# Kernel tuning notes

Hardware: AMD Instinct MI355X
Metric: run time of the kernel (lower is better)

Reference implementation:

```python
import jax, jax.numpy as jnp
import numpy as np

N_NODES = 50000
NEG_SLOPE = 0.2

def _gat_conv(x, W, att_src, att_dst, bias, src, dst):
    # x: [N, in_c] -> h: [N, out_c]
    h = x @ W
    a_src = (h * att_src).sum(-1)  # [N]
    a_dst = (h * att_dst).sum(-1)  # [N]
    e = a_src[src] + a_dst[dst]    # [E]
    e = jnp.where(e > 0, e, NEG_SLOPE * e)  # LeakyReLU
    # segment softmax over destination node neighborhoods
    emax = jax.ops.segment_max(e, dst, num_segments=N_NODES)
    ee = jnp.exp(e - emax[dst])
    denom = jax.ops.segment_sum(ee, dst, num_segments=N_NODES)
    alpha = ee / denom[dst]        # [E]
    out = jax.ops.segment_sum(h[src] * alpha[:, None], dst, num_segments=N_NODES)
    return out + bias

def _with_self_loops(edge_index):
    # PyG GATConv default add_self_loops=True
    loop = jnp.arange(N_NODES, dtype=edge_index.dtype)
    src = jnp.concatenate([edge_index[0], loop])
    dst = jnp.concatenate([edge_index[1], loop])
    return src, dst

def setup_inputs() -> dict:
    key = jax.random.key(0)
    ks = jax.random.split(key, 11)
    in_c, hid_c, out_c = 256, 128, 64
    E = 800000
    x = jax.random.normal(ks[0], (N_NODES, in_c), dtype=jnp.float32)
    edge_index = jax.random.randint(ks[1], (2, E), 0, N_NODES, dtype=jnp.int64)
    s1 = 1.0 / np.sqrt(in_c)
    s2 = 1.0 / np.sqrt(hid_c)
    return {
        "x": x,
        "edge_index": edge_index,
        "W1": jax.random.normal(ks[2], (in_c, hid_c), dtype=jnp.float32) * s1,
        "att_src1": jax.random.normal(ks[3], (hid_c,), dtype=jnp.float32) * s2,
        "att_dst1": jax.random.normal(ks[4], (hid_c,), dtype=jnp.float32) * s2,
        "b1": jax.random.normal(ks[5], (hid_c,), dtype=jnp.float32) * 0.01,
        "W2": jax.random.normal(ks[6], (hid_c, out_c), dtype=jnp.float32) * s2,
        "att_src2": jax.random.normal(ks[7], (out_c,), dtype=jnp.float32) * (1.0 / np.sqrt(out_c)),
        "att_dst2": jax.random.normal(ks[8], (out_c,), dtype=jnp.float32) * (1.0 / np.sqrt(out_c)),
        "b2": jax.random.normal(ks[9], (out_c,), dtype=jnp.float32) * 0.01,
    }

def reference(x, edge_index, W1, att_src1, att_dst1, b1, W2, att_src2, att_dst2, b2):
    src, dst = _with_self_loops(edge_index)
    hid = _gat_conv(x, W1, att_src1, att_dst1, b1, src, dst)
    hid = jax.nn.relu(hid)
    out = _gat_conv(hid, W2, att_src2, att_dst2, b2, src, dst)
    return jax.nn.log_softmax(out, axis=1)
```

## Files before the change

### kernel.cpp

```cpp
#include <hip/hip_runtime.h>
#include <hip/hip_bf16.h>
#include <math.h>

#define N_NODES 50000
#define E_RAW   800000
#define E_TOT   850000
#define NEG_SLOPE 0.2f
#define CAP 64

typedef __attribute__((ext_vector_type(8))) short short8;
typedef __attribute__((ext_vector_type(4))) float f32x4;

__device__ __forceinline__ short f2bf(float f) {
    __hip_bfloat16 h = __float2bfloat16(f);
    return *reinterpret_cast<short*>(&h);
}
__device__ __forceinline__ unsigned int f2bfu(float f) {
    __hip_bfloat16 h = __float2bfloat16(f);
    return (unsigned int)*reinterpret_cast<unsigned short*>(&h);
}
__device__ __forceinline__ float bflo(unsigned int u) {
    return __uint_as_float(u << 16);
}
__device__ __forceinline__ float bfhi(unsigned int u) {
    return __uint_as_float(u & 0xffff0000u);
}

template<int K, int N>
__global__ __launch_bounds__(256) void gat_wf_kernel(
        const float* __restrict__ W, short* __restrict__ Wf) {
    constexpr int NT = N / 16;
    const int idx = blockIdx.x * 256 + threadIdx.x;
    if (idx >= K * N) return;
    const int j  = idx & 7;
    const int n  = (idx >> 3) & 15;
    const int q  = (idx >> 7) & 3;
    const int t  = (idx >> 9) % NT;
    const int kc = idx / (512 * NT);
    const int k   = kc * 32 + q * 8 + j;
    const int col = t * 16 + n;
    Wf[idx] = f2bf(W[(size_t)k * N + col]);
}

template<int K, int N, bool BF16_IN>
__device__ __forceinline__ void gemm_att_body(
        const int blk,
        const float* __restrict__ xf, const short* __restrict__ xb,
        const short* __restrict__ Wf,
        const float* __restrict__ att_src, const float* __restrict__ att_dst,
        short* __restrict__ h_bf,
        float* __restrict__ a_src, float* __restrict__ a_dst) {
    constexpr int NT = N / 16;
    constexpr int KC = K / 32;
    const int tid  = threadIdx.x;
    const int lane = tid & 63;
    const int wv   = tid >> 6;
    const int mrow = lane & 15;
    const int q    = lane >> 4;

    const int row0 = blk * 64 + wv * 16;
    const int rowA = row0 + mrow;
    const int rowAc = rowA < N_NODES ? rowA : 0;

    f32x4 acc[NT];
    #pragma unroll
    for (int t = 0; t < NT; ++t) acc[t] = f32x4{0.f, 0.f, 0.f, 0.f};

    #pragma unroll
    for (int kc = 0; kc < KC; ++kc) {
        short8 a;
        if (BF16_IN) {
            a = *(const short8*)&xb[(size_t)rowAc * K + kc * 32 + q * 8];
        } else {
            const float4 f0 = *(const float4*)&xf[(size_t)rowAc * K + kc * 32 + q * 8];
            const float4 f1 = *(const float4*)&xf[(size_t)rowAc * K + kc * 32 + q * 8 + 4];
            a[0] = f2bf(f0.x); a[1] = f2bf(f0.y); a[2] = f2bf(f0.z); a[3] = f2bf(f0.w);
            a[4] = f2bf(f1.x); a[5] = f2bf(f1.y); a[6] = f2bf(f1.z); a[7] = f2bf(f1.w);
        }
        #pragma unroll
        for (int t = 0; t < NT; ++t) {
            const short8 b = *(const short8*)&Wf[((size_t)(kc * NT + t) * 64 + lane) * 8];
            acc[t] = __builtin_amdgcn_mfma_f32_16x16x32_bf16(a, b, acc[t], 0, 0, 0);
        }
    }

    #pragma unroll
    for (int r = 0; r < 4; ++r) {
        const int rowD = row0 + q * 4 + r;
        float ps = 0.0f, pd = 0.0f;
        #pragma unroll
        for (int t = 0; t < NT; ++t) {
            const int col = t * 16 + mrow;
            ps = fmaf(acc[t][r], att_src[col], ps);
            pd = fmaf(acc[t][r], att_dst[col], pd);
        }
        #pragma unroll
        for (int off = 8; off > 0; off >>= 1) {
            ps += __shfl_xor(ps, off);
            pd += __shfl_xor(pd, off);
        }
        if (rowD < N_NODES) {
            if (mrow == 0) { a_src[rowD] = ps; a_dst[rowD] = pd; }
            #pragma unroll
            for (int t = 0; t < NT; ++t)
                h_bf[(size_t)rowD * N + t * 16 + mrow] = f2bf(acc[t][r]);
        }
    }
}

template<int K, int N>
__global__ __launch_bounds__(256) void gat_fat1_kernel(
        const float* __restrict__ xf, const short* __restrict__ Wf,
        const float* __restrict__ att_src, const float* __restrict__ att_dst,
        short* __restrict__ h_bf,
        float* __restrict__ a_src, float* __restrict__ a_dst,
        const int* __restrict__ ei, int* __restrict__ cnt,
        int* __restrict__ srcs, int GB) {
    if ((int)blockIdx.x < GB) {
        gemm_att_body<K, N, false>(blockIdx.x, xf, nullptr, Wf,
                                   att_src, att_dst, h_bf, a_src, a_dst);
    } else {
        const int i = (blockIdx.x - GB) * 256 + threadIdx.x;
        if (i >= E_TOT) return;
        int s, d;
        if (i < E_RAW) { s = ei[i]; d = ei[E_RAW + i]; }
        else           { s = d = i - E_RAW; }
        const int c = atomicAdd(&cnt[d], 1);
        if (c < CAP) srcs[(d << 6) + c] = s;
    }
}

template<int K, int N, bool BF16_IN>
__global__ __launch_bounds__(256) void gat_gemm_att_kernel(
        const float* __restrict__ xf, const short* __restrict__ xb,
        const short* __restrict__ Wf,
        const float* __restrict__ att_src, const float* __restrict__ att_dst,
        short* __restrict__ h_bf,
        float* __restrict__ a_src, float* __restrict__ a_dst) {
    gemm_att_body<K, N, BF16_IN>(blockIdx.x, xf, xb, Wf,
                                 att_src, att_dst, h_bf, a_src, a_dst);
}

template<int N, bool RELU, bool LSM, bool OUT_BF16>
__global__ __launch_bounds__(256) void gat_aggr_kernel(
        const int* __restrict__ cnt, const int* __restrict__ srcs,
        const float* __restrict__ a_src, const float* __restrict__ a_dst,
        const unsigned short* __restrict__ h_bf, const float* __restrict__ bias,
        float* __restrict__ outf, uint4* __restrict__ outb) {
    constexpr int EPL = N / 16;
    const int lane = threadIdx.x & 63;
    const int wave = threadIdx.x >> 6;
    const int d = blockIdx.x * 4 + wave;
    if (d >= N_NODES) return;
    const int beg = d << 6;
    int deg = cnt[d];
    deg = deg < CAP ? deg : CAP;
    const float ad = a_dst[d];

    const int sreg = srcs[beg + (lane < deg ? lane : 0)];
    float e;
    if (lane < deg) {
        float t = a_src[sreg] + ad;
        e = t > 0.0f ? t : NEG_SLOPE * t;
    } else {
        e = -1e30f;
    }
    float m = e;
    #pragma unroll
    for (int off = 32; off > 0; off >>= 1) m = fmaxf(m, __shfl_xor(m, off));
    const float anum = __expf(e - m);
    float ss = anum;
    #pragma unroll
    for (int off = 32; off > 0; off >>= 1) ss += __shfl_xor(ss, off);
    const float areg = anum / ss;

    const int g   = lane >> 4;
    const int sub = lane & 15;
    float acc[EPL];
    #pragma unroll
    for (int c = 0; c < EPL; ++c) acc[c] = 0.0f;

    for (int j = 0; j < deg; j += 4) {
        const int eidx = j + g;
        const int s    = __shfl(sreg, eidx);
        float alpha    = __shfl(areg, eidx);
        if (eidx >= deg) alpha = 0.0f;
        const unsigned short* hp = h_bf + (size_t)s * N + sub * EPL;
        if (EPL == 8) {
            const uint4 hv = *(const uint4*)hp;
            acc[0] = fmaf(alpha, bflo(hv.x), acc[0]);
            acc[1] = fmaf(alpha, bfhi(hv.x), acc[1]);
            acc[2] = fmaf(alpha, bflo(hv.y), acc[2]);
            acc[3] = fmaf(alpha, bfhi(hv.y), acc[3]);
            acc[4] = fmaf(alpha, bflo(hv.z), acc[4]);
            acc[5] = fmaf(alpha, bfhi(hv.z), acc[5]);
            acc[6] = fmaf(alpha, bflo(hv.w), acc[6]);
            acc[7] = fmaf(alpha, bfhi(hv.w), acc[7]);
        } else {
            const uint2 hv = *(const uint2*)hp;
            acc[0] = fmaf(alpha, bflo(hv.x), acc[0]);
            acc[1] = fmaf(alpha, bfhi(hv.x), acc[1]);
            acc[2] = fmaf(alpha, bflo(hv.y), acc[2]);
            acc[3] = fmaf(alpha, bfhi(hv.y), acc[3]);
        }
    }

    #pragma unroll
    for (int c = 0; c < EPL; ++c) {
        acc[c] += __shfl_xor(acc[c], 16);
        acc[c] += __shfl_xor(acc[c], 32);
    }

    if (LSM) {
        float v[4];
        #pragma unroll
        for (int c = 0; c < 4; ++c) v[c] = acc[c] + bias[sub * 4 + c];
        float mm = fmaxf(fmaxf(v[0], v[1]), fmaxf(v[2], v[3]));
        #pragma unroll
        for (int off = 1; off < 16; off <<= 1) mm = fmaxf(mm, __shfl_xor(mm, off));
        float es = __expf(v[0] - mm) + __expf(v[1] - mm)
                 + __expf(v[2] - mm) + __expf(v[3] - mm);
        #pragma unroll
        for (int off = 1; off < 16; off <<= 1) es += __shfl_xor(es, off);
        const float ls = logf(es);
        if (lane < 16) {
            float4 o;
            o.x = v[0] - mm - ls; o.y = v[1] - mm - ls;
            o.z = v[2] - mm - ls; o.w = v[3] - mm - ls;
            *(float4*)&outf[(size_t)d * N + sub * 4] = o;
        }
    } else {
        if (lane < 16) {
            const float4 b0 = *(const float4*)&bias[sub * 8];
            const float4 b1 = *(const float4*)&bias[sub * 8 + 4];
            float v[8];
            v[0] = acc[0] + b0.x; v[1] = acc[1] + b0.y;
            v[2] = acc[2] + b0.z; v[3] = acc[3] + b0.w;
            v[4] = acc[4] + b1.x; v[5] = acc[5] + b1.y;
            v[6] = acc[6] + b1.z; v[7] = acc[7] + b1.w;
            if (RELU)
                #pragma unroll
                for (int c = 0; c < 8; ++c) v[c] = fmaxf(v[c], 0.0f);
            uint4 p;
            p.x = f2bfu(v[0]) | (f2bfu(v[1]) << 16);
            p.y = f2bfu(v[2]) | (f2bfu(v[3]) << 16);
            p.z = f2bfu(v[4]) | (f2bfu(v[5]) << 16);
            p.w = f2bfu(v[6]) | (f2bfu(v[7]) << 16);
            outb[(size_t)d * (N / 8) + sub] = p;
        }
    }
}

extern "C" void kernel_launch(void* const* d_in, const int* in_sizes, int n_in,
                              void* d_out, int out_size, void* d_ws, size_t ws_size,
                              hipStream_t stream) {
    const float* x        = (const float*)d_in[0];
    const int*   ei       = (const int*)  d_in[1];
    const float* W1       = (const float*)d_in[2];
    const float* att_src1 = (const float*)d_in[3];
    const float* att_dst1 = (const float*)d_in[4];
    const float* b1       = (const float*)d_in[5];
    const float* W2       = (const float*)d_in[6];
    const float* att_src2 = (const float*)d_in[7];
    const float* att_dst2 = (const float*)d_in[8];
    const float* b2       = (const float*)d_in[9];
    float* out = (float*)d_out;
    float* ws  = (float*)d_ws;

    float* a_src1 = ws;
    float* a_dst1 = a_src1 + 50000;
    float* a_src2 = a_dst1 + 50000;
    float* a_dst2 = a_src2 + 50000;
    int*   cnt    = (int*)(a_dst2 + 50000);
    int*   srcs   = cnt + 50000;
    short* hbf1   = (short*)(srcs + 50000 * CAP);
    short* agg1b  = hbf1  + 6400000;
    short* Wf1    = agg1b + 6400000;
    short* Wf2    = Wf1   + 32768;
    short* hbf2   = hbf1;

    hipMemsetAsync(cnt, 0, (size_t)50000 * 4, stream);

    const int EB = (E_TOT + 255) / 256;
    const int GB = (N_NODES + 63) / 64;

    gat_wf_kernel<256, 128><<<128, 256, 0, stream>>>(W1, Wf1);
    gat_wf_kernel<128, 64><<<32, 256, 0, stream>>>(W2, Wf2);

    gat_fat1_kernel<256, 128><<<GB + EB, 256, 0, stream>>>(
        x, Wf1, att_src1, att_dst1, hbf1, a_src1, a_dst1,
        ei, cnt, srcs, GB);

    gat_aggr_kernel<128, true, false, true><<<12500, 256, 0, stream>>>(
        cnt, srcs, a_src1, a_dst1, (const unsigned short*)hbf1, b1,
        nullptr, (uint4*)agg1b);

    gat_gemm_att_kernel<128, 64, true><<<GB, 256, 0, stream>>>(
        nullptr, agg1b, Wf2, att_src2, att_dst2, hbf2, a_src2, a_dst2);
    gat_aggr_kernel<64, false, true, false><<<12500, 256, 0, stream>>>(
        cnt, srcs, a_src2, a_dst2, (const unsigned short*)hbf2, b2,
        out, nullptr);
}
```

Before: 245.9 us.

## Process more edges per wave iteration in aggregation and merge weight-prep launches

The aggregation kernel now has each lane own 16 feature columns and load two 16-byte chunks per edge. This lets a wave handle 8 edges per iteration for the 128-wide layer and 16 for the 64-wide layer, instead of 4. The goal is fewer serial loop trips and more memory loads in flight per gathered row. In exchange it needs a longer cross-lane reduction and more accumulator registers. The two weight-conversion launches are also merged into one kernel to save a launch.

After: 260.7 us. 6.0% more time.

```diff
diff --git a/kernel.cpp b/kernel.cpp
--- a/kernel.cpp
+++ b/kernel.cpp
@@ -27,10 +27,10 @@
 }
 
 template<int K, int N>
-__global__ __launch_bounds__(256) void gat_wf_kernel(
-        const float* __restrict__ W, short* __restrict__ Wf) {
+__device__ __forceinline__ void wf_body(
+        int blk, const float* __restrict__ W, short* __restrict__ Wf) {
     constexpr int NT = N / 16;
-    const int idx = blockIdx.x * 256 + threadIdx.x;
+    const int idx = blk * 256 + threadIdx.x;
     if (idx >= K * N) return;
     const int j  = idx & 7;
     const int n  = (idx >> 3) & 15;
@@ -40,6 +40,14 @@
     const int k   = kc * 32 + q * 8 + j;
     const int col = t * 16 + n;
     Wf[idx] = f2bf(W[(size_t)k * N + col]);
+}
+
+__global__ __launch_bounds__(256) void gat_wf2x_kernel(
+        const float* __restrict__ W1, short* __restrict__ Wf1,
+        const float* __restrict__ W2, short* __restrict__ Wf2) {
+    const int b = blockIdx.x;
+    if (b < 128) wf_body<256, 128>(b, W1, Wf1);
+    else         wf_body<128, 64>(b - 128, W2, Wf2);
 }
 
 template<int K, int N, bool BF16_IN>
@@ -141,13 +149,13 @@
                                  att_src, att_dst, h_bf, a_src, a_dst);
 }
 
-template<int N, bool RELU, bool LSM, bool OUT_BF16>
+template<int N, int SLOTS, bool LSM>
 __global__ __launch_bounds__(256) void gat_aggr_kernel(
         const int* __restrict__ cnt, const int* __restrict__ srcs,
         const float* __restrict__ a_src, const float* __restrict__ a_dst,
         const unsigned short* __restrict__ h_bf, const float* __restrict__ bias,
         float* __restrict__ outf, uint4* __restrict__ outb) {
-    constexpr int EPL = N / 16;
+    constexpr int LPR = 64 / SLOTS;
     const int lane = threadIdx.x & 63;
     const int wave = threadIdx.x >> 6;
     const int d = blockIdx.x * 4 + wave;
@@ -174,79 +182,88 @@
     for (int off = 32; off > 0; off >>= 1) ss += __shfl_xor(ss, off);
     const float areg = anum / ss;
 
-    const int g   = lane >> 4;
-    const int sub = lane & 15;
-    float acc[EPL];
-    #pragma unroll
-    for (int c = 0; c < EPL; ++c) acc[c] = 0.0f;
-
-    for (int j = 0; j < deg; j += 4) {
+    const int g = lane / LPR;
+    const int p = lane % LPR;
+    float acc[16];
+    #pragma unroll
+    for (int c = 0; c < 16; ++c) acc[c] = 0.0f;
+
+    for (int j = 0; j < deg; j += SLOTS) {
         const int eidx = j + g;
-        const int s    = __shfl(sreg, eidx);
-        float alpha    = __shfl(areg, eidx);
+        const int s    = __shfl(sreg, eidx & 63);
+        float alpha    = __shfl(areg, eidx & 63);
         if (eidx >= deg) alpha = 0.0f;
-        const unsigned short* hp = h_bf + (size_t)s * N + sub * EPL;
-        if (EPL == 8) {
-            const uint4 hv = *(const uint4*)hp;
-            acc[0] = fmaf(alpha, bflo(hv.x), acc[0]);
-            acc[1] = fmaf(alpha, bfhi(hv.x), acc[1]);
-            acc[2] = fmaf(alpha, bflo(hv.y), acc[2]);
-            acc[3] = fmaf(alpha, bfhi(hv.y), acc[3]);
-            acc[4] = fmaf(alpha, bflo(hv.z), acc[4]);
-            acc[5] = fmaf(alpha, bfhi(hv.z), acc[5]);
-            acc[6] = fmaf(alpha, bflo(hv.w), acc[6]);
-            acc[7] = fmaf(alpha, bfhi(hv.w), acc[7]);
-        } else {
-            const uint2 hv = *(const uint2*)hp;
-            acc[0] = fmaf(alpha, bflo(hv.x), acc[0]);
-            acc[1] = fmaf(alpha, bfhi(hv.x), acc[1]);
-            acc[2] = fmaf(alpha, bflo(hv.y), acc[2]);
-            acc[3] = fmaf(alpha, bfhi(hv.y), acc[3]);
-        }
-    }
-
-    #pragma unroll
-    for (int c = 0; c < EPL; ++c) {
-        acc[c] += __shfl_xor(acc[c], 16);
-        acc[c] += __shfl_xor(acc[c], 32);
+        const unsigned short* hp = h_bf + (size_t)s * N + p * 16;
+        const uint4 h0 = *(const uint4*)hp;
+        const uint4 h1 = *(const uint4*)(hp + 8);
+        acc[0]  = fmaf(alpha, bflo(h0.x), acc[0]);
+        acc[1]  = fmaf(alpha, bfhi(h0.x), acc[1]);
+        acc[2]  = fmaf(alpha, bflo(h0.y), acc[2]);
+        acc[3]  = fmaf(alpha, bfhi(h0.y), acc[3]);
+        acc[4]  = fmaf(alpha, bflo(h0.z), acc[4]);
+        acc[5]  = fmaf(alpha, bfhi(h0.z), acc[5]);
+        acc[6]  = fmaf(alpha, bflo(h0.w), acc[6]);
+        acc[7]  = fmaf(alpha, bfhi(h0.w), acc[7]);
+        acc[8]  = fmaf(alpha, bflo(h1.x), acc[8]);
+        acc[9]  = fmaf(alpha, bfhi(h1.x), acc[9]);
+        acc[10] = fmaf(alpha, bflo(h1.y), acc[10]);
+        acc[11] = fmaf(alpha, bfhi(h1.y), acc[11]);
+        acc[12] = fmaf(alpha, bflo(h1.z), acc[12]);
+        acc[13] = fmaf(alpha, bfhi(h1.z), acc[13]);
+        acc[14] = fmaf(alpha, bflo(h1.w), acc[14]);
+        acc[15] = fmaf(alpha, bfhi(h1.w), acc[15]);
+    }
+
+    #pragma unroll
+    for (int c = 0; c < 16; ++c) {
+        #pragma unroll
+        for (int off = LPR; off < 64; off <<= 1)
+            acc[c] += __shfl_xor(acc[c], off);
     }
 
     if (LSM) {
-        float v[4];
-        #pragma unroll
-        for (int c = 0; c < 4; ++c) v[c] = acc[c] + bias[sub * 4 + c];
-        float mm = fmaxf(fmaxf(v[0], v[1]), fmaxf(v[2], v[3]));
-        #pragma unroll
-        for (int off = 1; off < 16; off <<= 1) mm = fmaxf(mm, __shfl_xor(mm, off));
-        float es = __expf(v[0] - mm) + __expf(v[1] - mm)
-                 + __expf(v[2] - mm) + __expf(v[3] - mm);
-        #pragma unroll
-        for (int off = 1; off < 16; off <<= 1) es += __shfl_xor(es, off);
-        const float ls = logf(es);
-        if (lane < 16) {
-            float4 o;
-            o.x = v[0] - mm - ls; o.y = v[1] - mm - ls;
-            o.z = v[2] - mm - ls; o.w = v[3] - mm - ls;
-            *(float4*)&outf[(size_t)d * N + sub * 4] = o;
+        float v[16];
+        #pragma unroll
+        for (int c = 0; c < 16; ++c) v[c] = acc[c] + bias[p * 16 + c];
+        float mm = v[0];
+        #pragma unroll
+        for (int c = 1; c < 16; ++c) mm = fmaxf(mm, v[c]);
+        mm = fmaxf(mm, __shfl_xor(mm, 1));
+        mm = fmaxf(mm, __shfl_xor(mm, 2));
+        float es = 0.0f;
+        #pragma unroll
+        for (int c = 0; c < 16; ++c) es += __expf(v[c] - mm);
+        es += __shfl_xor(es, 1);
+        es += __shfl_xor(es, 2);
+        const float ls = mm + logf(es);
+        if (lane < 4) {
+            #pragma unroll
+            for (int i = 0; i < 4; ++i) {
+                float4 o;
+                o.x = v[i * 4 + 0] - ls; o.y = v[i * 4 + 1] - ls;
+                o.z = v[i * 4 + 2] - ls; o.w = v[i * 4 + 3] - ls;
+                *(float4*)&outf[(size_t)d * N + p * 16 + i * 4] = o;
+            }
         }
     } else {
-        if (lane < 16) {
-            const float4 b0 = *(const float4*)&bias[sub * 8];
-            const float4 b1 = *(const float4*)&bias[sub * 8 + 4];
-            float v[8];
-            v[0] = acc[0] + b0.x; v[1] = acc[1] + b0.y;
-            v[2] = acc[2] + b0.z; v[3] = acc[3] + b0.w;
-            v[4] = acc[4] + b1.x; v[5] = acc[5] + b1.y;
-            v[6] = acc[6] + b1.z; v[7] = acc[7] + b1.w;
-            if (RELU)
-                #pragma unroll
-                for (int c = 0; c < 8; ++c) v[c] = fmaxf(v[c], 0.0f);
-            uint4 p;
-            p.x = f2bfu(v[0]) | (f2bfu(v[1]) << 16);
-            p.y = f2bfu(v[2]) | (f2bfu(v[3]) << 16);
-            p.z = f2bfu(v[4]) | (f2bfu(v[5]) << 16);
-            p.w = f2bfu(v[6]) | (f2bfu(v[7]) << 16);
-            outb[(size_t)d * (N / 8) + sub] = p;
+        if (lane < 8) {
+            float v[16];
+            #pragma unroll
+            for (int c = 0; c < 16; ++c) {
+                v[c] = acc[c] + bias[p * 16 + c];
+                v[c] = fmaxf(v[c], 0.0f);
+            }
+            uint4 pk0, pk1;
+            pk0.x = f2bfu(v[0])  | (f2bfu(v[1])  << 16);
+            pk0.y = f2bfu(v[2])  | (f2bfu(v[3])  << 16);
+            pk0.z = f2bfu(v[4])  | (f2bfu(v[5])  << 16);
+            pk0.w = f2bfu(v[6])  | (f2bfu(v[7])  << 16);
+            pk1.x = f2bfu(v[8])  | (f2bfu(v[9])  << 16);
+            pk1.y = f2bfu(v[10]) | (f2bfu(v[11]) << 16);
+            pk1.z = f2bfu(v[12]) | (f2bfu(v[13]) << 16);
+            pk1.w = f2bfu(v[14]) | (f2bfu(v[15]) << 16);
+            outb[(size_t)d * 16 + p * 2]     = pk0;
+            outb[(size_t)d * 16 + p * 2 + 1] = pk1;
         }
     }
 }
@@ -284,20 +301,19 @@
     const int EB = (E_TOT + 255) / 256;
     const int GB = (N_NODES + 63) / 64;
 
-    gat_wf_kernel<256, 128><<<128, 256, 0, stream>>>(W1, Wf1);
-    gat_wf_kernel<128, 64><<<32, 256, 0, stream>>>(W2, Wf2);
+    gat_wf2x_kernel<<<160, 256, 0, stream>>>(W1, Wf1, W2, Wf2);
 
     gat_fat1_kernel<256, 128><<<GB + EB, 256, 0, stream>>>(
         x, Wf1, att_src1, att_dst1, hbf1, a_src1, a_dst1,
         ei, cnt, srcs, GB);
 
-    gat_aggr_kernel<128, true, false, true><<<12500, 256, 0, stream>>>(
+    gat_aggr_kernel<128, 8, false><<<12500, 256, 0, stream>>>(
         cnt, srcs, a_src1, a_dst1, (const unsigned short*)hbf1, b1,
         nullptr, (uint4*)agg1b);
 
     gat_gemm_att_kernel<128, 64, true><<<GB, 256, 0, stream>>>(
         nullptr, agg1b, Wf2, att_src2, att_dst2, hbf2, a_src2, a_dst2);
-    gat_aggr_kernel<64, false, true, false><<<12500, 256, 0, stream>>>(
+    gat_aggr_kernel<64, 16, true><<<12500, 256, 0, stream>>>(
         cnt, srcs, a_src2, a_dst2, (const unsigned short*)hbf2, b2,
         out, nullptr);
 }
```
